# Kernel optimization log

Measured on AMD Instinct MI355X. Metric: run time of the kernel, lower is better.

Reference implementation:

```python
import jax, jax.numpy as jnp
import numpy as np

N, E, IN, HID, HEADS, OUT = 20000, 320000, 128, 64, 8, 64
NEG_SLOPE = 0.2  # PyG GATConv default leaky_relu slope


def setup_inputs() -> dict:
    key = jax.random.key(0)
    ks = jax.random.split(key, 12)
    g = lambda k, shape, fan_in: jax.random.normal(k, shape, jnp.float32) / np.sqrt(fan_in)
    return {
        "x": jax.random.normal(ks[0], (N, IN), jnp.float32),
        "edge_index": jax.random.randint(ks[1], (2, E), 0, N, jnp.int32),
        "W1": g(ks[2], (IN, HEADS * HID), IN),
        "att_src1": g(ks[3], (HEADS, HID), HID),
        "att_dst1": g(ks[4], (HEADS, HID), HID),
        "b1": jnp.zeros((HEADS * HID,), jnp.float32),
        "W2": g(ks[5], (HEADS * HID, OUT), HEADS * HID),
        "att_src2": g(ks[6], (1, OUT), OUT),
        "att_dst2": g(ks[7], (1, OUT), OUT),
        "b2": jnp.zeros((OUT,), jnp.float32),
    }


def gat_conv(x, edge_index, W, att_src, att_dst, b, heads, out_ch):
    """PyG-style GATConv with add_self_loops=True, concat=True."""
    n = x.shape[0]
    loop = jnp.arange(n, dtype=edge_index.dtype)
    src = jnp.concatenate([edge_index[0], loop])  # message source nodes
    dst = jnp.concatenate([edge_index[1], loop])  # aggregation targets

    h = (x @ W).reshape(n, heads, out_ch)               # [N,H,C]
    a_s = jnp.sum(h * att_src[None], axis=-1)            # [N,H]
    a_d = jnp.sum(h * att_dst[None], axis=-1)            # [N,H]

    e = jax.nn.leaky_relu(a_s[src] + a_d[dst], NEG_SLOPE)  # [Etot,H]
    # numerically stable edge-softmax over incoming neighborhoods
    m = jax.ops.segment_max(e, dst, num_segments=n)
    m = jnp.where(jnp.isfinite(m), m, 0.0)
    p = jnp.exp(e - m[dst])
    denom = jax.ops.segment_sum(p, dst, num_segments=n)
    alpha = p / denom[dst]                               # [Etot,H]

    out = jax.ops.segment_sum(h[src] * alpha[:, :, None], dst, num_segments=n)  # [N,H,C]
    return out.reshape(n, heads * out_ch) + b


def reference(x, edge_index, W1, att_src1, att_dst1, b1, W2, att_src2, att_dst2, b2):
    h = gat_conv(x, edge_index, W1, att_src1, att_dst1, b1, HEADS, HID)
    h = jax.nn.relu(h)
    out = gat_conv(h, edge_index, W2, att_src2, att_dst2, b2, 1, OUT)
    return out
```

## Files before the change

kernel.cpp:

```cpp
#include <hip/hip_runtime.h>
#include <cstdint>

#define N_NODES 20000
#define N_EDGES 320000
#define ET (N_EDGES + N_NODES)
#define IN_DIM 128
#define HID 64
#define HEADS 8
#define F1 (HEADS * HID)
#define OUT_DIM 64
#define NEG_SLOPE 0.2f
#define NB_SCAN 20

typedef __attribute__((ext_vector_type(8))) short bf16x8;
typedef __attribute__((ext_vector_type(4))) float f32x4;

__device__ __forceinline__ ushort f2bf(float f) {
  uint32_t u = __float_as_uint(f);
  uint32_t r = (u + 0x7fffu + ((u >> 16) & 1u)) >> 16;
  return (ushort)r;
}
__device__ __forceinline__ float bfu_lo(uint32_t p) { return __uint_as_float(p << 16); }
__device__ __forceinline__ float bfu_hi(uint32_t p) { return __uint_as_float(p & 0xffff0000u); }
__device__ __forceinline__ float lrelu(float x) { return x > 0.f ? x : NEG_SLOPE * x; }

__global__ void prep_kernel(const float* __restrict__ x, const float* __restrict__ W1,
                            const float* __restrict__ W2, ushort* __restrict__ xb,
                            ushort* __restrict__ W1T, ushort* __restrict__ W2T) {
  const int NX4 = N_NODES * IN_DIM / 4;
  int idx = blockIdx.x * 256 + threadIdx.x;
  if (idx < NX4) {
    float4 v = reinterpret_cast<const float4*>(x)[idx];
    ushort4 o;
    o.x = f2bf(v.x); o.y = f2bf(v.y); o.z = f2bf(v.z); o.w = f2bf(v.w);
    reinterpret_cast<ushort4*>(xb)[idx] = o;
  } else if (idx < NX4 + IN_DIM * F1) {
    int k = idx - NX4;
    int r = k / F1, c = k - r * F1;
    W1T[(size_t)c * IN_DIM + r] = f2bf(W1[k]);
  } else if (idx < NX4 + IN_DIM * F1 + F1 * OUT_DIM) {
    int k = idx - NX4 - IN_DIM * F1;
    int r = k / OUT_DIM, c = k - r * OUT_DIM;
    W2T[(size_t)c * F1 + r] = f2bf(W2[k]);
  }
}

__global__ void hist_kernel(const int* __restrict__ ei, int* __restrict__ deg) {
  int e = blockIdx.x * 256 + threadIdx.x;
  if (e >= ET) return;
  int dst = (e < N_EDGES) ? ei[N_EDGES + e] : (e - N_EDGES);
  atomicAdd(&deg[dst], 1);
}

__global__ __launch_bounds__(1024) void scan_a(const int* __restrict__ deg,
                                               int* __restrict__ off,
                                               int* __restrict__ bsum) {
  __shared__ int wsum[16];
  int i = blockIdx.x * 1024 + threadIdx.x;
  int lane = threadIdx.x & 63, wid = threadIdx.x >> 6;
  int v = (i < N_NODES) ? deg[i] : 0;
  int s = v;
#pragma unroll
  for (int d = 1; d < 64; d <<= 1) {
    int u = __shfl_up(s, d);
    if (lane >= d) s += u;
  }
  if (lane == 63) wsum[wid] = s;
  __syncthreads();
  if (wid == 0) {
    int ws = (lane < 16) ? wsum[lane] : 0;
#pragma unroll
    for (int d = 1; d < 16; d <<= 1) {
      int u = __shfl_up(ws, d);
      if (lane >= d) ws += u;
    }
    if (lane < 16) wsum[lane] = ws;
  }
  __syncthreads();
  int wbase = (wid > 0) ? wsum[wid - 1] : 0;
  int incl = wbase + s;
  if (i < N_NODES) off[i] = incl - v;
  if (threadIdx.x == 1023) bsum[blockIdx.x] = incl;
}

__global__ void scan_b(const int* __restrict__ bsum, int* __restrict__ boff,
                       int* __restrict__ off) {
  int lane = threadIdx.x;
  int orig = (lane < NB_SCAN) ? bsum[lane] : 0;
  int v = orig;
#pragma unroll
  for (int d = 1; d < 64; d <<= 1) {
    int u = __shfl_up(v, d);
    if (lane >= d) v += u;
  }
  if (lane < NB_SCAN) boff[lane] = v - orig;
  if (lane == NB_SCAN - 1) off[N_NODES] = v;
}

__global__ __launch_bounds__(1024) void scan_c(const int* __restrict__ boff,
                                               int* __restrict__ off,
                                               int* __restrict__ pos) {
  int i = blockIdx.x * 1024 + threadIdx.x;
  if (i >= N_NODES) return;
  int o = off[i] + boff[blockIdx.x];
  off[i] = o;
  pos[i] = o;
}

__global__ void scatter_kernel(const int* __restrict__ ei, int* __restrict__ pos,
                               int* __restrict__ csr_src) {
  int e = blockIdx.x * 256 + threadIdx.x;
  if (e >= ET) return;
  int src, dst;
  if (e < N_EDGES) { src = ei[e]; dst = ei[N_EDGES + e]; }
  else             { src = e - N_EDGES; dst = src; }
  int slot = atomicAdd(&pos[dst], 1);
  csr_src[slot] = src;
}

__device__ __forceinline__ int swz(int r, int kg) { return kg ^ ((r >> 1) & 3); }

template <int WR, int WC, int TM, int TN, int ASD>
__global__ __launch_bounds__(256) void gemm_kernel(
    const ushort* __restrict__ A, const ushort* __restrict__ BT,
    ushort* __restrict__ Cb, int M, int K, int NC,
    const float* __restrict__ atts, const float* __restrict__ attd,
    float* __restrict__ asd) {
  constexpr int BM = WR * TM * 16;
  constexpr int BN = WC * TN * 16;
  __shared__ ushort As[BM * 32];
  __shared__ ushort Bs[BN * 32];
  const int t = threadIdx.x;
  const int lane = t & 63, wid = t >> 6;
  const int wr = wid / WC, wc = wid % WC;
  const int m0 = blockIdx.y * BM, n0 = blockIdx.x * BN;
  f32x4 acc[TM][TN] = {};
  const int srow = t >> 2, kg = t & 3;

  for (int k0 = 0; k0 < K; k0 += 32) {
#pragma unroll
    for (int q = 0; q < BM / 64; ++q) {
      int r = srow + 64 * q;
      int gr = m0 + r; if (gr >= M) gr = M - 1;
      bf16x8 v = *reinterpret_cast<const bf16x8*>(&A[(size_t)gr * K + k0 + kg * 8]);
      *reinterpret_cast<bf16x8*>(&As[r * 32 + swz(r, kg) * 8]) = v;
    }
#pragma unroll
    for (int q = 0; q < BN / 64; ++q) {
      int r = srow + 64 * q;
      int gn = n0 + r;
      bf16x8 v = *reinterpret_cast<const bf16x8*>(&BT[(size_t)gn * K + k0 + kg * 8]);
      *reinterpret_cast<bf16x8*>(&Bs[r * 32 + swz(r, kg) * 8]) = v;
    }
    __syncthreads();
    int kq = lane >> 4;
    int rr = lane & 15;
    bf16x8 af[TM], bfv[TN];
#pragma unroll
    for (int i = 0; i < TM; ++i) {
      int r = (wr * TM + i) * 16 + rr;
      af[i] = *reinterpret_cast<const bf16x8*>(&As[r * 32 + swz(r, kq) * 8]);
    }
#pragma unroll
    for (int j = 0; j < TN; ++j) {
      int r = (wc * TN + j) * 16 + rr;
      bfv[j] = *reinterpret_cast<const bf16x8*>(&Bs[r * 32 + swz(r, kq) * 8]);
    }
#pragma unroll
    for (int i = 0; i < TM; ++i)
#pragma unroll
      for (int j = 0; j < TN; ++j)
        acc[i][j] = __builtin_amdgcn_mfma_f32_16x16x32_bf16(af[i], bfv[j], acc[i][j], 0, 0, 0);
    __syncthreads();
  }
  const int cr0 = (lane >> 4) * 4;
  const int cc = lane & 15;
#pragma unroll
  for (int i = 0; i < TM; ++i)
#pragma unroll
    for (int j = 0; j < TN; ++j)
#pragma unroll
      for (int r = 0; r < 4; ++r) {
        int gm = m0 + (wr * TM + i) * 16 + cr0 + r;
        int gn = n0 + (wc * TN + j) * 16 + cc;
        if (gm < M) Cb[(size_t)gm * NC + gn] = f2bf(acc[i][j][r]);
      }
  if constexpr (ASD != 0) {
    static_assert(TN * 16 == 64, "asd fusion needs 64-col wave tile");
    const int hh = (ASD == 1) ? ((n0 + wc * 64) >> 6) : 0;
    float as_v[TN], ad_v[TN];
#pragma unroll
    for (int j = 0; j < TN; ++j) {
      as_v[j] = atts[hh * 64 + j * 16 + cc];
      ad_v[j] = attd[hh * 64 + j * 16 + cc];
    }
#pragma unroll
    for (int i = 0; i < TM; ++i)
#pragma unroll
      for (int r = 0; r < 4; ++r) {
        float ps = 0.f, pd = 0.f;
#pragma unroll
        for (int j = 0; j < TN; ++j) {
          ps += acc[i][j][r] * as_v[j];
          pd += acc[i][j][r] * ad_v[j];
        }
#pragma unroll
        for (int s = 1; s < 16; s <<= 1) {
          ps += __shfl_xor(ps, s);
          pd += __shfl_xor(pd, s);
        }
        int row = m0 + (wr * TM + i) * 16 + cr0 + r;
        if (cc == 0 && row < M) {
          if constexpr (ASD == 1) {
            asd[(size_t)row * 16 + hh] = ps;
            asd[(size_t)row * 16 + 8 + hh] = pd;
          } else {
            asd[(size_t)row * 2 + 0] = ps;
            asd[(size_t)row * 2 + 1] = pd;
          }
        }
      }
  }
}

__global__ __launch_bounds__(64) void agg1_kernel(
    const int* __restrict__ off, const int* __restrict__ csrs,
    const float* __restrict__ asd, const ushort* __restrict__ H1b,
    const float* __restrict__ b1, ushort* __restrict__ X2b) {
  __shared__ float w_lds[64];
  __shared__ int src_lds[16];
  int bid = blockIdx.x;
  int phase = (bid >= N_NODES) ? 1 : 0;
  int node = bid - phase * N_NODES;
  int lane = threadIdx.x;
  int hl = lane >> 4, j = lane & 15;
  int head = phase * 4 + hl;
  int s0 = off[node], s1 = off[node + 1];
  float adst = asd[(size_t)node * 16 + 8 + head];
  const uint2* Hp = reinterpret_cast<const uint2*>(H1b);
  const int uoff = head * 16 + j;
  float m = -1e30f, s = 0.f;
  float a0 = 0.f, a1 = 0.f, a2 = 0.f, a3 = 0.f;
  for (int c0 = s0; c0 < s1; c0 += 16) {
    int n = s1 - c0; if (n > 16) n = 16;
    int src = (j < n) ? csrs[c0 + j] : 0;
    if (lane < 16) src_lds[lane] = src;
    float e = (j < n) ? lrelu(asd[(size_t)src * 16 + head] + adst) : -1e30f;
    float mc = e;
#pragma unroll
    for (int d = 1; d < 16; d <<= 1) mc = fmaxf(mc, __shfl_xor(mc, d));
    float mn = fmaxf(m, mc);
    float wv = (j < n) ? __expf(e - mn) : 0.f;
    float ws = wv;
#pragma unroll
    for (int d = 1; d < 16; d <<= 1) ws += __shfl_xor(ws, d);
    float r = __expf(m - mn);
    s = s * r + ws;
    a0 *= r; a1 *= r; a2 *= r; a3 *= r;
    m = mn;
    w_lds[lane] = wv;
    int i = 0;
    for (; i + 2 <= n; i += 2) {
      int sA = src_lds[i], sB = src_lds[i + 1];
      float wA = w_lds[hl * 16 + i], wB = w_lds[hl * 16 + i + 1];
      uint2 pA = Hp[(size_t)sA * 128 + uoff];
      uint2 pB = Hp[(size_t)sB * 128 + uoff];
      a0 += wA * bfu_lo(pA.x) + wB * bfu_lo(pB.x);
      a1 += wA * bfu_hi(pA.x) + wB * bfu_hi(pB.x);
      a2 += wA * bfu_lo(pA.y) + wB * bfu_lo(pB.y);
      a3 += wA * bfu_hi(pA.y) + wB * bfu_hi(pB.y);
    }
    if (i < n) {
      int sA = src_lds[i];
      float wA = w_lds[hl * 16 + i];
      uint2 p = Hp[(size_t)sA * 128 + uoff];
      a0 += wA * bfu_lo(p.x); a1 += wA * bfu_hi(p.x);
      a2 += wA * bfu_lo(p.y); a3 += wA * bfu_hi(p.y);
    }
  }
  float inv = 1.f / s;
  int fb = head * 64 + j * 4;
  float v0 = fmaxf(a0 * inv + b1[fb], 0.f);
  float v1 = fmaxf(a1 * inv + b1[fb + 1], 0.f);
  float v2 = fmaxf(a2 * inv + b1[fb + 2], 0.f);
  float v3 = fmaxf(a3 * inv + b1[fb + 3], 0.f);
  uint2 o;
  o.x = (uint32_t)f2bf(v0) | ((uint32_t)f2bf(v1) << 16);
  o.y = (uint32_t)f2bf(v2) | ((uint32_t)f2bf(v3) << 16);
  reinterpret_cast<uint2*>(X2b)[(size_t)node * 128 + uoff] = o;
}

__global__ __launch_bounds__(256) void agg2_kernel(
    const int* __restrict__ off, const int* __restrict__ csrs,
    const float* __restrict__ asd, const ushort* __restrict__ H2b,
    const float* __restrict__ b2, float* __restrict__ out) {
  __shared__ float w_lds[4][64];
  __shared__ int src_lds[4][64];
  int wv_id = threadIdx.x >> 6;
  int node = blockIdx.x * 4 + wv_id;
  if (node >= N_NODES) return;
  int lane = threadIdx.x & 63;
  int grp = lane >> 4, fr = lane & 15;
  int s0 = off[node], s1 = off[node + 1];
  float adst = asd[(size_t)node * 2 + 1];
  const uint2* Hp = reinterpret_cast<const uint2*>(H2b);
  float m = -1e30f, s = 0.f;
  float a0 = 0.f, a1 = 0.f, a2 = 0.f, a3 = 0.f;
  for (int c0 = s0; c0 < s1; c0 += 64) {
    int n = s1 - c0; if (n > 64) n = 64;
    int src = (lane < n) ? csrs[c0 + lane] : 0;
    float e = (lane < n) ? lrelu(asd[(size_t)src * 2] + adst) : -1e30f;
    float mc = e;
#pragma unroll
    for (int d = 1; d < 64; d <<= 1) mc = fmaxf(mc, __shfl_xor(mc, d));
    float mn = fmaxf(m, mc);
    float wv = (lane < n) ? __expf(e - mn) : 0.f;
    float ws = wv;
#pragma unroll
    for (int d = 1; d < 64; d <<= 1) ws += __shfl_xor(ws, d);
    float r = __expf(m - mn);
    s = s * r + ws;
    a0 *= r; a1 *= r; a2 *= r; a3 *= r;
    m = mn;
    src_lds[wv_id][lane] = src;
    w_lds[wv_id][lane] = wv;
    int i = grp;
    for (; i + 4 < n; i += 8) {
      int sA = src_lds[wv_id][i], sB = src_lds[wv_id][i + 4];
      float wA = w_lds[wv_id][i], wB = w_lds[wv_id][i + 4];
      uint2 pA = Hp[(size_t)sA * 16 + fr];
      uint2 pB = Hp[(size_t)sB * 16 + fr];
      a0 += wA * bfu_lo(pA.x) + wB * bfu_lo(pB.x);
      a1 += wA * bfu_hi(pA.x) + wB * bfu_hi(pB.x);
      a2 += wA * bfu_lo(pA.y) + wB * bfu_lo(pB.y);
      a3 += wA * bfu_hi(pA.y) + wB * bfu_hi(pB.y);
    }
    if (i < n) {
      int sA = src_lds[wv_id][i];
      float wA = w_lds[wv_id][i];
      uint2 p = Hp[(size_t)sA * 16 + fr];
      a0 += wA * bfu_lo(p.x); a1 += wA * bfu_hi(p.x);
      a2 += wA * bfu_lo(p.y); a3 += wA * bfu_hi(p.y);
    }
  }
#pragma unroll
  for (int d = 16; d < 64; d <<= 1) {
    a0 += __shfl_xor(a0, d);
    a1 += __shfl_xor(a1, d);
    a2 += __shfl_xor(a2, d);
    a3 += __shfl_xor(a3, d);
  }
  if (grp == 0) {
    float inv = 1.f / s;
    int fb = fr * 4;
    float4 o;
    o.x = a0 * inv + b2[fb];
    o.y = a1 * inv + b2[fb + 1];
    o.z = a2 * inv + b2[fb + 2];
    o.w = a3 * inv + b2[fb + 3];
    reinterpret_cast<float4*>(out)[(size_t)node * 16 + fr] = o;
  }
}

extern "C" void kernel_launch(void* const* d_in, const int* in_sizes, int n_in,
                              void* d_out, int out_size, void* d_ws, size_t ws_size,
                              hipStream_t stream) {
  const float* x        = (const float*)d_in[0];
  const int*   ei       = (const int*)  d_in[1];
  const float* W1       = (const float*)d_in[2];
  const float* att_src1 = (const float*)d_in[3];
  const float* att_dst1 = (const float*)d_in[4];
  const float* b1       = (const float*)d_in[5];
  const float* W2       = (const float*)d_in[6];
  const float* att_src2 = (const float*)d_in[7];
  const float* att_dst2 = (const float*)d_in[8];
  const float* b2       = (const float*)d_in[9];
  float* out = (float*)d_out;

  char* w = (char*)d_ws;
  auto alloc = [&](size_t bytes) {
    char* p = w;
    w += (bytes + 255) & ~(size_t)255;
    return p;
  };
  ushort* xb     = (ushort*)alloc((size_t)N_NODES * IN_DIM * 2);
  ushort* W1T    = (ushort*)alloc((size_t)F1 * IN_DIM * 2);
  ushort* W2T    = (ushort*)alloc((size_t)OUT_DIM * F1 * 2);
  ushort* H1b    = (ushort*)alloc((size_t)N_NODES * F1 * 2);
  ushort* X2b    = (ushort*)alloc((size_t)N_NODES * F1 * 2);
  ushort* H2b    = (ushort*)alloc((size_t)N_NODES * OUT_DIM * 2);
  float* asd1    = (float*)alloc((size_t)N_NODES * 16 * 4);
  float* asd2    = (float*)alloc((size_t)N_NODES * 2 * 4);
  int* deg       = (int*)alloc((size_t)N_NODES * 4);
  int* off       = (int*)alloc((size_t)(N_NODES + 1) * 4);
  int* pos       = (int*)alloc((size_t)N_NODES * 4);
  int* csrsrc    = (int*)alloc((size_t)ET * 4);
  int* bsum      = (int*)alloc((size_t)NB_SCAN * 4);
  int* boff      = (int*)alloc((size_t)NB_SCAN * 4);

  hipMemsetAsync(deg, 0, (size_t)N_NODES * 4, stream);
  hist_kernel<<<(ET + 255) / 256, 256, 0, stream>>>(ei, deg);
  scan_a<<<NB_SCAN, 1024, 0, stream>>>(deg, off, bsum);
  scan_b<<<1, 64, 0, stream>>>(bsum, boff, off);
  scan_c<<<NB_SCAN, 1024, 0, stream>>>(boff, off, pos);
  scatter_kernel<<<(ET + 255) / 256, 256, 0, stream>>>(ei, pos, csrsrc);

  {
    int total = N_NODES * IN_DIM / 4 + IN_DIM * F1 + F1 * OUT_DIM;
    prep_kernel<<<(total + 255) / 256, 256, 0, stream>>>(x, W1, W2, xb, W1T, W2T);
  }

  gemm_kernel<2, 2, 4, 4, 1>
      <<<dim3(F1 / 128, (N_NODES + 127) / 128), 256, 0, stream>>>(
      xb, W1T, H1b, N_NODES, IN_DIM, F1, att_src1, att_dst1, asd1);
  agg1_kernel<<<2 * N_NODES, 64, 0, stream>>>(off, csrsrc, asd1, H1b, b1, X2b);

  gemm_kernel<4, 1, 1, 4, 2>
      <<<dim3(1, (N_NODES + 63) / 64), 256, 0, stream>>>(
      X2b, W2T, H2b, N_NODES, F1, OUT_DIM, att_src2, att_dst2, asd2);
  agg2_kernel<<<(N_NODES + 3) / 4, 256, 0, stream>>>(off, csrsrc, asd2, H2b, b2, out);
}
```

Baseline: 144.6 us.

## Remap agg1 to one head per block with four nodes per wave

The layer-1 aggregation kernel previously gave each block one node and four heads, two blocks per node. Now each 64-thread block handles one head for four different nodes, one 16-lane group per node. Source indices and softmax weights are broadcast with wave shuffles instead of LDS. The intent is to drop the LDS round-trips and balance load across nodes with different degrees, at the cost of divergent loop trip counts inside a wave and a scattered, head-strided gather pattern.

```diff
diff --git a/kernel.cpp b/kernel.cpp
--- a/kernel.cpp
+++ b/kernel.cpp
@@ -227,30 +227,27 @@
     const int* __restrict__ off, const int* __restrict__ csrs,
     const float* __restrict__ asd, const ushort* __restrict__ H1b,
     const float* __restrict__ b1, ushort* __restrict__ X2b) {
-  __shared__ float w_lds[64];
-  __shared__ int src_lds[16];
   int bid = blockIdx.x;
-  int phase = (bid >= N_NODES) ? 1 : 0;
-  int node = bid - phase * N_NODES;
+  int head = bid & 7;
+  int nb = bid >> 3;
   int lane = threadIdx.x;
-  int hl = lane >> 4, j = lane & 15;
-  int head = phase * 4 + hl;
+  int grp = lane >> 4, fr = lane & 15;
+  int gb = grp << 4;
+  int node = nb * 4 + grp;
   int s0 = off[node], s1 = off[node + 1];
   float adst = asd[(size_t)node * 16 + 8 + head];
-  const uint2* Hp = reinterpret_cast<const uint2*>(H1b);
-  const int uoff = head * 16 + j;
+  const uint2* Hh = reinterpret_cast<const uint2*>(H1b) + head * 16 + fr;
   float m = -1e30f, s = 0.f;
   float a0 = 0.f, a1 = 0.f, a2 = 0.f, a3 = 0.f;
   for (int c0 = s0; c0 < s1; c0 += 16) {
-    int n = s1 - c0; if (n > 16) n = 16;
-    int src = (j < n) ? csrs[c0 + j] : 0;
-    if (lane < 16) src_lds[lane] = src;
-    float e = (j < n) ? lrelu(asd[(size_t)src * 16 + head] + adst) : -1e30f;
+    int nn = s1 - c0; if (nn > 16) nn = 16;
+    int src_f = (fr < nn) ? csrs[c0 + fr] : 0;
+    float e = (fr < nn) ? lrelu(asd[(size_t)src_f * 16 + head] + adst) : -1e30f;
     float mc = e;
 #pragma unroll
     for (int d = 1; d < 16; d <<= 1) mc = fmaxf(mc, __shfl_xor(mc, d));
     float mn = fmaxf(m, mc);
-    float wv = (j < n) ? __expf(e - mn) : 0.f;
+    float wv = (fr < nn) ? __expf(e - mn) : 0.f;
     float ws = wv;
 #pragma unroll
     for (int d = 1; d < 16; d <<= 1) ws += __shfl_xor(ws, d);
@@ -258,28 +255,29 @@
     s = s * r + ws;
     a0 *= r; a1 *= r; a2 *= r; a3 *= r;
     m = mn;
-    w_lds[lane] = wv;
     int i = 0;
-    for (; i + 2 <= n; i += 2) {
-      int sA = src_lds[i], sB = src_lds[i + 1];
-      float wA = w_lds[hl * 16 + i], wB = w_lds[hl * 16 + i + 1];
-      uint2 pA = Hp[(size_t)sA * 128 + uoff];
-      uint2 pB = Hp[(size_t)sB * 128 + uoff];
+    for (; i + 2 <= nn; i += 2) {
+      int sA = __shfl(src_f, gb + i);
+      int sB = __shfl(src_f, gb + i + 1);
+      float wA = __shfl(wv, gb + i);
+      float wB = __shfl(wv, gb + i + 1);
+      uint2 pA = Hh[(size_t)sA * 128];
+      uint2 pB = Hh[(size_t)sB * 128];
       a0 += wA * bfu_lo(pA.x) + wB * bfu_lo(pB.x);
       a1 += wA * bfu_hi(pA.x) + wB * bfu_hi(pB.x);
       a2 += wA * bfu_lo(pA.y) + wB * bfu_lo(pB.y);
       a3 += wA * bfu_hi(pA.y) + wB * bfu_hi(pB.y);
     }
-    if (i < n) {
-      int sA = src_lds[i];
-      float wA = w_lds[hl * 16 + i];
-      uint2 p = Hp[(size_t)sA * 128 + uoff];
+    if (i < nn) {
+      int sA = __shfl(src_f, gb + i);
+      float wA = __shfl(wv, gb + i);
+      uint2 p = Hh[(size_t)sA * 128];
       a0 += wA * bfu_lo(p.x); a1 += wA * bfu_hi(p.x);
       a2 += wA * bfu_lo(p.y); a3 += wA * bfu_hi(p.y);
     }
   }
   float inv = 1.f / s;
-  int fb = head * 64 + j * 4;
+  int fb = head * 64 + fr * 4;
   float v0 = fmaxf(a0 * inv + b1[fb], 0.f);
   float v1 = fmaxf(a1 * inv + b1[fb + 1], 0.f);
   float v2 = fmaxf(a2 * inv + b1[fb + 2], 0.f);
@@ -287,7 +285,7 @@
   uint2 o;
   o.x = (uint32_t)f2bf(v0) | ((uint32_t)f2bf(v1) << 16);
   o.y = (uint32_t)f2bf(v2) | ((uint32_t)f2bf(v3) << 16);
-  reinterpret_cast<uint2*>(X2b)[(size_t)node * 128 + uoff] = o;
+  reinterpret_cast<uint2*>(X2b)[(size_t)node * 128 + head * 16 + fr] = o;
 }
 
 __global__ __launch_bounds__(256) void agg2_kernel(
@@ -413,7 +411,7 @@
   gemm_kernel<2, 2, 4, 4, 1>
       <<<dim3(F1 / 128, (N_NODES + 127) / 128), 256, 0, stream>>>(
       xb, W1T, H1b, N_NODES, IN_DIM, F1, att_src1, att_dst1, asd1);
-  agg1_kernel<<<2 * N_NODES, 64, 0, stream>>>(off, csrsrc, asd1, H1b, b1, X2b);
+  agg1_kernel<<<HEADS * (N_NODES / 4), 64, 0, stream>>>(off, csrsrc, asd1, H1b, b1, X2b);
 
   gemm_kernel<4, 1, 1, 4, 2>
       <<<dim3(1, (N_NODES + 63) / 64), 256, 0, stream>>>(
```

After: 143.7 us. About the same (-0.6%).
